# Kernel optimization log

Hardware: AMD Instinct MI355X
Metric: run time of the kernel (lower is better)

## Reference

```python
import jax, jax.numpy as jnp
import numpy as np

N = 50000       # nodes
E = 800000      # edges (avg degree 16)
D_IN = 128      # in_channels
H = 128         # hidden_channels
C = 10          # num_classes
G = 64          # graphs in batch


def setup_inputs() -> dict:
    key = jax.random.key(0)
    ks = jax.random.split(key, 9)
    x = jax.random.normal(ks[0], (N, D_IN), dtype=jnp.float32)
    edge_index = jax.random.randint(ks[1], (2, E), 0, N, dtype=jnp.int32)
    batch = jnp.sort(jax.random.randint(ks[2], (N,), 0, G, dtype=jnp.int32))
    # glorot-ish init for weights, zeros for biases (PyG GCNConv default: glorot W, zero b)
    W1 = jax.random.normal(ks[3], (D_IN, H), dtype=jnp.float32) * (1.0 / np.sqrt(D_IN))
    b1 = jnp.zeros((H,), dtype=jnp.float32)
    W2 = jax.random.normal(ks[4], (H, H), dtype=jnp.float32) * (1.0 / np.sqrt(H))
    b2 = jnp.zeros((H,), dtype=jnp.float32)
    Wc = jax.random.normal(ks[5], (H, C), dtype=jnp.float32) * (1.0 / np.sqrt(H))
    bc = jnp.zeros((C,), dtype=jnp.float32)
    return {"x": x, "edge_index": edge_index, "batch": batch,
            "W1": W1, "b1": b1, "W2": W2, "b2": b2, "Wc": Wc, "bc": bc}


def _gcn_conv(x, edge_index, W, b):
    # PyG GCNConv: add self-loops, symmetric normalization D^-1/2 (A+I) D^-1/2 (X W) + b
    loop = jnp.arange(N, dtype=edge_index.dtype)
    row = jnp.concatenate([edge_index[0], loop])  # source
    col = jnp.concatenate([edge_index[1], loop])  # target (aggregation side)
    deg = jax.ops.segment_sum(jnp.ones(row.shape[0], dtype=x.dtype), col, num_segments=N)
    dis = jax.lax.rsqrt(deg)  # deg >= 1 due to self-loops
    norm = dis[row] * dis[col]                     # [E+N]
    h = x @ W                                      # [N, H]
    msg = h[row] * norm[:, None]                   # gather + scale
    out = jax.ops.segment_sum(msg, col, num_segments=N)  # scatter-add at targets
    return out + b


def reference(x, edge_index, batch, W1, b1, W2, b2, Wc, bc):
    h = jax.nn.relu(_gcn_conv(x, edge_index, W1, b1))
    h = jax.nn.relu(_gcn_conv(h, edge_index, W2, b2))
    # global mean pool per graph
    sums = jax.ops.segment_sum(h, batch, num_segments=G)          # [G, H]
    counts = jax.ops.segment_sum(jnp.ones((N,), dtype=h.dtype), batch, num_segments=G)
    pooled = sums / jnp.maximum(counts, 1.0)[:, None]
    return pooled @ Wc + bc                                       # [G, C]
```

## Files before the change

### kernel.cpp

```cpp
#include <hip/hip_runtime.h>
#include <hip/hip_fp16.h>

typedef _Float16 half8 __attribute__((ext_vector_type(8)));
typedef float f32x4 __attribute__((ext_vector_type(4)));

#define PAD 64


__global__ __launch_bounds__(256) void fill_pad_k(const int* __restrict__ row, const int* __restrict__ col,
                                                  int* __restrict__ cnt, unsigned short* __restrict__ csr,
                                                  int E) {
    int i8 = blockIdx.x * 256 + threadIdx.x;
    int base = i8 * 8;
    if (base + 7 < E) {
        int4 r0 = ((const int4*)row)[i8 * 2];
        int4 r1 = ((const int4*)row)[i8 * 2 + 1];
        int4 c0 = ((const int4*)col)[i8 * 2];
        int4 c1 = ((const int4*)col)[i8 * 2 + 1];
        int p0 = atomicAdd(&cnt[c0.x], 1);
        int p1 = atomicAdd(&cnt[c0.y], 1);
        int p2 = atomicAdd(&cnt[c0.z], 1);
        int p3 = atomicAdd(&cnt[c0.w], 1);
        int p4 = atomicAdd(&cnt[c1.x], 1);
        int p5 = atomicAdd(&cnt[c1.y], 1);
        int p6 = atomicAdd(&cnt[c1.z], 1);
        int p7 = atomicAdd(&cnt[c1.w], 1);
        if (p0 < PAD) csr[c0.x * PAD + p0] = (unsigned short)r0.x;
        if (p1 < PAD) csr[c0.y * PAD + p1] = (unsigned short)r0.y;
        if (p2 < PAD) csr[c0.z * PAD + p2] = (unsigned short)r0.z;
        if (p3 < PAD) csr[c0.w * PAD + p3] = (unsigned short)r0.w;
        if (p4 < PAD) csr[c1.x * PAD + p4] = (unsigned short)r1.x;
        if (p5 < PAD) csr[c1.y * PAD + p5] = (unsigned short)r1.y;
        if (p6 < PAD) csr[c1.z * PAD + p6] = (unsigned short)r1.z;
        if (p7 < PAD) csr[c1.w * PAD + p7] = (unsigned short)r1.w;
    } else {
        for (int e = base; e < E; ++e) {
            int t = col[e];
            int p = atomicAdd(&cnt[t], 1);
            if (p < PAD) csr[t * PAD + p] = (unsigned short)row[e];
        }
    }
}

__global__ __launch_bounds__(256) void dis_k(const int* __restrict__ cnt, float* __restrict__ dis, int n) {
    int i = blockIdx.x * 256 + threadIdx.x;
    if (i < n) dis[i] = rsqrtf(1.0f + (float)min(cnt[i], PAD));
}


template<bool FP16IN>
__global__ __launch_bounds__(256) void gemm_mfma(const void* __restrict__ Ain,
                                                 const float* __restrict__ W,
                                                 const float* __restrict__ dis,
                                                 _Float16* __restrict__ O, int nrows) {
    int tid = threadIdx.x;
    int lane = tid & 63;
    int wave = tid >> 6;
    int wr = wave >> 1, wc = wave & 1;
    int row0 = blockIdx.x * 64 + wr * 32;
    int colbase = wc * 64;
    int lrow = lane & 15;
    int lkb = lane >> 4;

    half8 bfrag[4][4];
    #pragma unroll
    for (int ct = 0; ct < 4; ++ct) {
        int colw = colbase + ct * 16 + lrow;
        #pragma unroll
        for (int ks = 0; ks < 4; ++ks) {
            int k0 = ks * 32 + lkb * 8;
            #pragma unroll
            for (int j = 0; j < 8; ++j)
                bfrag[ct][ks][j] = (_Float16)W[(k0 + j) * 128 + colw];
        }
    }

    f32x4 acc[2][4] = {};
    #pragma unroll
    for (int ks = 0; ks < 4; ++ks) {
        int k0 = ks * 32 + lkb * 8;
        half8 afrag[2];
        #pragma unroll
        for (int rt = 0; rt < 2; ++rt) {
            int r = row0 + rt * 16 + lrow;
            r = r < nrows ? r : nrows - 1;
            if (FP16IN) {
                afrag[rt] = *reinterpret_cast<const half8*>(&((const _Float16*)Ain)[r * 128 + k0]);
            } else {
                const float4* p = reinterpret_cast<const float4*>(&((const float*)Ain)[r * 128 + k0]);
                float4 u = p[0], v = p[1];
                half8 h;
                h[0] = (_Float16)u.x; h[1] = (_Float16)u.y; h[2] = (_Float16)u.z; h[3] = (_Float16)u.w;
                h[4] = (_Float16)v.x; h[5] = (_Float16)v.y; h[6] = (_Float16)v.z; h[7] = (_Float16)v.w;
                afrag[rt] = h;
            }
        }
        #pragma unroll
        for (int rt = 0; rt < 2; ++rt)
            #pragma unroll
            for (int ct = 0; ct < 4; ++ct)
                acc[rt][ct] = __builtin_amdgcn_mfma_f32_16x16x32_f16(afrag[rt], bfrag[ct][ks],
                                                                     acc[rt][ct], 0, 0, 0);
    }

    #pragma unroll
    for (int rt = 0; rt < 2; ++rt) {
        #pragma unroll
        for (int j = 0; j < 4; ++j) {
            int r = row0 + rt * 16 + lkb * 4 + j;
            if (r < nrows) {
                float d = dis[r];
                #pragma unroll
                for (int ct = 0; ct < 4; ++ct) {
                    int colw = colbase + ct * 16 + lrow;
                    O[r * 128 + colw] = (_Float16)(acc[rt][ct][j] * d);
                }
            }
        }
    }
}


__device__ __forceinline__ float2 gather_sum(const __half2* __restrict__ h2,
                                             const unsigned short* __restrict__ src,
                                             int e, int lane, float2 a0) {
    float2 a1 = {0.f, 0.f}, a2 = {0.f, 0.f}, a3 = {0.f, 0.f};
    int i = 0;
    for (; i + 7 < e; i += 8) {
        int s0 = src[i],     s1 = src[i + 1], s2 = src[i + 2], s3 = src[i + 3];
        int s4 = src[i + 4], s5 = src[i + 5], s6 = src[i + 6], s7 = src[i + 7];
        float2 v0 = __half22float2(h2[s0 * 64 + lane]);
        float2 v1 = __half22float2(h2[s1 * 64 + lane]);
        float2 v2 = __half22float2(h2[s2 * 64 + lane]);
        float2 v3 = __half22float2(h2[s3 * 64 + lane]);
        float2 v4 = __half22float2(h2[s4 * 64 + lane]);
        float2 v5 = __half22float2(h2[s5 * 64 + lane]);
        float2 v6 = __half22float2(h2[s6 * 64 + lane]);
        float2 v7 = __half22float2(h2[s7 * 64 + lane]);
        a0.x += v0.x; a0.y += v0.y;
        a1.x += v1.x; a1.y += v1.y;
        a2.x += v2.x; a2.y += v2.y;
        a3.x += v3.x; a3.y += v3.y;
        a0.x += v4.x; a0.y += v4.y;
        a1.x += v5.x; a1.y += v5.y;
        a2.x += v6.x; a2.y += v6.y;
        a3.x += v7.x; a3.y += v7.y;
    }
    for (; i + 3 < e; i += 4) {
        int s0 = src[i], s1 = src[i + 1], s2 = src[i + 2], s3 = src[i + 3];
        float2 v0 = __half22float2(h2[s0 * 64 + lane]);
        float2 v1 = __half22float2(h2[s1 * 64 + lane]);
        float2 v2 = __half22float2(h2[s2 * 64 + lane]);
        float2 v3 = __half22float2(h2[s3 * 64 + lane]);
        a0.x += v0.x; a0.y += v0.y;
        a1.x += v1.x; a1.y += v1.y;
        a2.x += v2.x; a2.y += v2.y;
        a3.x += v3.x; a3.y += v3.y;
    }
    for (; i < e; ++i) {
        float2 v0 = __half22float2(h2[src[i] * 64 + lane]);
        a0.x += v0.x; a0.y += v0.y;
    }
    float2 r;
    r.x = a0.x + a1.x + a2.x + a3.x;
    r.y = a0.y + a1.y + a2.y + a3.y;
    return r;
}

__global__ __launch_bounds__(256) void agg_k(const _Float16* __restrict__ h, const int* __restrict__ cnt,
                                             const unsigned short* __restrict__ csr_pad,
                                             const float* __restrict__ dis,
                                             const float* __restrict__ bias,
                                             _Float16* __restrict__ out, int n) {
    int wave = threadIdx.x >> 6;
    int lane = threadIdx.x & 63;
    int node = blockIdx.x * 4 + wave;
    if (node >= n) return;
    const __half2* h2 = (const __half2*)h;
    float2 self = __half22float2(h2[node * 64 + lane]);
    int deg = min(cnt[node], PAD);
    float2 a = gather_sum(h2, csr_pad + node * PAD, deg, lane, self);
    float d = dis[node];
    float2 bb = ((const float2*)bias)[lane];
    float vx = a.x * d + bb.x;
    float vy = a.y * d + bb.y;
    ((__half2*)out)[node * 64 + lane] = __floats2half2_rn(fmaxf(vx, 0.f), fmaxf(vy, 0.f));
}


__global__ __launch_bounds__(256) void agg_pool_k(const _Float16* __restrict__ h,
                                                  const int* __restrict__ cnt,
                                                  const unsigned short* __restrict__ csr_pad,
                                                  const float* __restrict__ dis,
                                                  const float* __restrict__ bias,
                                                  const int* __restrict__ batch,
                                                  float* __restrict__ sums, int n) {
    int wave = threadIdx.x >> 6;
    int lane = threadIdx.x & 63;
    int node0 = (blockIdx.x * 4 + wave) * 4;
    if (node0 >= n) return;
    const __half2* h2 = (const __half2*)h;
    float2 bb = ((const float2*)bias)[lane];
    float2 pool = {0.f, 0.f};
    int curg = batch[node0];
    #pragma unroll
    for (int k = 0; k < 4; ++k) {
        int node = node0 + k;
        if (node >= n) break;
        float2 self = __half22float2(h2[node * 64 + lane]);
        int deg = min(cnt[node], PAD);
        float2 a = gather_sum(h2, csr_pad + node * PAD, deg, lane, self);
        float d = dis[node];
        float vx = fmaxf(a.x * d + bb.x, 0.f);
        float vy = fmaxf(a.y * d + bb.y, 0.f);
        int g = batch[node];
        if (g != curg) {
            atomicAdd(&sums[curg * 128 + lane * 2], pool.x);
            atomicAdd(&sums[curg * 128 + lane * 2 + 1], pool.y);
            pool.x = 0.f; pool.y = 0.f;
            curg = g;
        }
        pool.x += vx;
        pool.y += vy;
    }
    atomicAdd(&sums[curg * 128 + lane * 2], pool.x);
    atomicAdd(&sums[curg * 128 + lane * 2 + 1], pool.y);
}


__global__ __launch_bounds__(256) void bounds_k(const int* __restrict__ batch, int* __restrict__ start,
                                                int n, int g) {
    int i = blockIdx.x * 256 + threadIdx.x;
    if (i >= n) return;
    int b = batch[i];
    int bp = (i == 0) ? -1 : batch[i - 1];
    for (int q = bp + 1; q <= b; ++q) start[q] = i;
    if (i == n - 1) for (int q = b + 1; q <= g; ++q) start[q] = n;
}

__global__ __launch_bounds__(128) void final_k(const float* __restrict__ sums, const int* __restrict__ start,
                                               const float* __restrict__ Wc, const float* __restrict__ bc,
                                               float* __restrict__ outp, int C) {
    __shared__ float sp[128];
    int g = blockIdx.x;
    int t = threadIdx.x;
    float cntf = fmaxf((float)(start[g + 1] - start[g]), 1.0f);
    sp[t] = sums[g * 128 + t] / cntf;
    __syncthreads();
    if (t < C) {
        float acc = bc[t];
        #pragma unroll 8
        for (int cc = 0; cc < 128; ++cc) acc += sp[cc] * Wc[cc * C + t];
        outp[g * C + t] = acc;
    }
}


extern "C" void kernel_launch(void* const* d_in, const int* in_sizes, int n_in,
                              void* d_out, int out_size, void* d_ws, size_t ws_size,
                              hipStream_t stream) {
    const float* x    = (const float*)d_in[0];
    const int*   ei   = (const int*)d_in[1];
    const int*   batch= (const int*)d_in[2];
    const float* W1   = (const float*)d_in[3];
    const float* b1   = (const float*)d_in[4];
    const float* W2   = (const float*)d_in[5];
    const float* b2   = (const float*)d_in[6];
    const float* Wc   = (const float*)d_in[7];
    const float* bc   = (const float*)d_in[8];

    const int N = in_sizes[0] / 128;
    const int E = in_sizes[1] / 2;
    const int C = in_sizes[7] / 128;
    const int G = out_size / C;

    const int* row = ei;
    const int* col = ei + E;

    char* ws = (char*)d_ws;
    size_t o = 0;
    auto take = [&](size_t nbytes) -> char* {
        char* p = ws + o;
        o = (o + nbytes + 255) & ~(size_t)255;
        return p;
    };
    int*   cnt     = (int*)take((size_t)N * 4);
    float* sums    = (float*)take((size_t)G * 128 * 4);
    size_t zero_span = o;
    float* dis     = (float*)take((size_t)N * 4);
    int*   start   = (int*)take((size_t)(G + 1) * 4);
    unsigned short* csr_pad = (unsigned short*)take((size_t)N * PAD * 2);
    _Float16* bufA = (_Float16*)take((size_t)N * 128 * 2);
    _Float16* bufB = (_Float16*)take((size_t)N * 128 * 2);

    hipMemsetAsync(d_ws, 0, zero_span, stream);

    int gE8 = (E / 8 + 255) / 256;
    int gN = (N + 255) / 256;

    fill_pad_k<<<gE8, 256, 0, stream>>>(row, col, cnt, csr_pad, E);
    dis_k<<<gN, 256, 0, stream>>>(cnt, dis, N);

    int gGemm = (N + 63) / 64;
    int gAgg  = (N + 3) / 4;
    int gAggP = (N + 15) / 16;

    gemm_mfma<false><<<gGemm, 256, 0, stream>>>((const void*)x, W1, dis, bufA, N);
    agg_k<<<gAgg, 256, 0, stream>>>(bufA, cnt, csr_pad, dis, b1, bufB, N);
    gemm_mfma<true><<<gGemm, 256, 0, stream>>>((const void*)bufB, W2, dis, bufA, N);
    agg_pool_k<<<gAggP, 256, 0, stream>>>(bufA, cnt, csr_pad, dis, b2, batch, sums, N);

    bounds_k<<<gN, 256, 0, stream>>>(batch, start, N, G);
    final_k<<<G, 128, 0, stream>>>(sums, start, Wc, bc, (float*)d_out, C);
}
```

Baseline: 175.8 us.

## Gather rows with 16-byte vector loads over four nodes per wave

Both aggregation kernels now assign four nodes to each wave. Each 16-lane quarter handles an edge slot and loads 8 fp16 features at once with a 16-byte load. Partial sums are combined across lanes with xor shuffles. The self-loop is moved into the padded CSR as slot 0 by a new init kernel, and a zero row N serves as the target for masked-out edge slots. The aim is more memory-level parallelism and wider loads in the gather-bound aggregation. The cost is extra shuffle reductions and padded work up to the maximum degree in each group of four nodes. Putting the self-loop inside the 64-slot pad also means one fewer real neighbour fits per node.

Result: slower. 309.4 us (+76.0%).

```diff
diff --git a/kernel.cpp b/kernel.cpp
--- a/kernel.cpp
+++ b/kernel.cpp
@@ -1,10 +1,22 @@
 #include <hip/hip_runtime.h>
 #include <hip/hip_fp16.h>
 
+typedef _Float16 half8v __attribute__((ext_vector_type(8)));
+typedef float f32x4 __attribute__((ext_vector_type(4)));
 typedef _Float16 half8 __attribute__((ext_vector_type(8)));
-typedef float f32x4 __attribute__((ext_vector_type(4)));
 
 #define PAD 64
+
+
+__global__ __launch_bounds__(256) void csr_init_k(int* __restrict__ cnt, unsigned short* __restrict__ csr,
+                                                  _Float16* __restrict__ rowN, int n) {
+    int i = blockIdx.x * 256 + threadIdx.x;
+    if (i < n) {
+        cnt[i] = 1;
+        csr[(size_t)i * PAD] = (unsigned short)i;
+    }
+    if (blockIdx.x == 0 && threadIdx.x < 128) rowN[threadIdx.x] = (_Float16)0.f;
+}
 
 
 __global__ __launch_bounds__(256) void fill_pad_k(const int* __restrict__ row, const int* __restrict__ col,
@@ -44,7 +56,7 @@
 
 __global__ __launch_bounds__(256) void dis_k(const int* __restrict__ cnt, float* __restrict__ dis, int n) {
     int i = blockIdx.x * 256 + threadIdx.x;
-    if (i < n) dis[i] = rsqrtf(1.0f + (float)min(cnt[i], PAD));
+    if (i < n) dis[i] = rsqrtf((float)min(cnt[i], PAD));
 }
 
 
@@ -121,110 +133,132 @@
 }
 
 
-__device__ __forceinline__ float2 gather_sum(const __half2* __restrict__ h2,
-                                             const unsigned short* __restrict__ src,
-                                             int e, int lane, float2 a0) {
-    float2 a1 = {0.f, 0.f}, a2 = {0.f, 0.f}, a3 = {0.f, 0.f};
-    int i = 0;
-    for (; i + 7 < e; i += 8) {
-        int s0 = src[i],     s1 = src[i + 1], s2 = src[i + 2], s3 = src[i + 3];
-        int s4 = src[i + 4], s5 = src[i + 5], s6 = src[i + 6], s7 = src[i + 7];
-        float2 v0 = __half22float2(h2[s0 * 64 + lane]);
-        float2 v1 = __half22float2(h2[s1 * 64 + lane]);
-        float2 v2 = __half22float2(h2[s2 * 64 + lane]);
-        float2 v3 = __half22float2(h2[s3 * 64 + lane]);
-        float2 v4 = __half22float2(h2[s4 * 64 + lane]);
-        float2 v5 = __half22float2(h2[s5 * 64 + lane]);
-        float2 v6 = __half22float2(h2[s6 * 64 + lane]);
-        float2 v7 = __half22float2(h2[s7 * 64 + lane]);
-        a0.x += v0.x; a0.y += v0.y;
-        a1.x += v1.x; a1.y += v1.y;
-        a2.x += v2.x; a2.y += v2.y;
-        a3.x += v3.x; a3.y += v3.y;
-        a0.x += v4.x; a0.y += v4.y;
-        a1.x += v5.x; a1.y += v5.y;
-        a2.x += v6.x; a2.y += v6.y;
-        a3.x += v7.x; a3.y += v7.y;
-    }
-    for (; i + 3 < e; i += 4) {
-        int s0 = src[i], s1 = src[i + 1], s2 = src[i + 2], s3 = src[i + 3];
-        float2 v0 = __half22float2(h2[s0 * 64 + lane]);
-        float2 v1 = __half22float2(h2[s1 * 64 + lane]);
-        float2 v2 = __half22float2(h2[s2 * 64 + lane]);
-        float2 v3 = __half22float2(h2[s3 * 64 + lane]);
-        a0.x += v0.x; a0.y += v0.y;
-        a1.x += v1.x; a1.y += v1.y;
-        a2.x += v2.x; a2.y += v2.y;
-        a3.x += v3.x; a3.y += v3.y;
-    }
-    for (; i < e; ++i) {
-        float2 v0 = __half22float2(h2[src[i] * 64 + lane]);
-        a0.x += v0.x; a0.y += v0.y;
-    }
-    float2 r;
-    r.x = a0.x + a1.x + a2.x + a3.x;
-    r.y = a0.y + a1.y + a2.y + a3.y;
-    return r;
-}
+__device__ __forceinline__ void gather4(const _Float16* __restrict__ h,
+                                        const unsigned short* __restrict__ csr,
+                                        const int* __restrict__ cnt,
+                                        int node0, int n, int q, int p,
+                                        float acc[4][8]) {
+    int deg[4];
+    const unsigned short* base[4];
+    #pragma unroll
+    for (int j = 0; j < 4; ++j) {
+        int nd = node0 + j;
+        bool v = nd < n;
+        deg[j] = v ? min(cnt[nd], PAD) : 0;
+        base[j] = csr + (size_t)(v ? nd : 0) * PAD;
+    }
+    int maxdeg = max(max(deg[0], deg[1]), max(deg[2], deg[3]));
+    for (int i = 0; i < maxdeg; i += 8) {
+        #pragma unroll
+        for (int j = 0; j < 4; ++j) {
+            int ea = i + q, eb = i + 4 + q;
+            int ia = base[j][ea];
+            int ib = base[j][eb];
+            ia = ea < deg[j] ? ia : n;
+            ib = eb < deg[j] ? ib : n;
+            half8v va = *reinterpret_cast<const half8v*>(h + (size_t)ia * 128 + p * 8);
+            half8v vb = *reinterpret_cast<const half8v*>(h + (size_t)ib * 128 + p * 8);
+            #pragma unroll
+            for (int c = 0; c < 8; ++c)
+                acc[j][c] += (float)va[c] + (float)vb[c];
+        }
+    }
+}
+
+__device__ __forceinline__ void reduce8(float a[8]) {
+    #pragma unroll
+    for (int c = 0; c < 8; ++c) {
+        float t = a[c];
+        t += __shfl_xor(t, 16);
+        t += __shfl_xor(t, 32);
+        a[c] = t;
+    }
+}
+
 
 __global__ __launch_bounds__(256) void agg_k(const _Float16* __restrict__ h, const int* __restrict__ cnt,
-                                             const unsigned short* __restrict__ csr_pad,
+                                             const unsigned short* __restrict__ csr,
                                              const float* __restrict__ dis,
                                              const float* __restrict__ bias,
                                              _Float16* __restrict__ out, int n) {
     int wave = threadIdx.x >> 6;
     int lane = threadIdx.x & 63;
-    int node = blockIdx.x * 4 + wave;
-    if (node >= n) return;
-    const __half2* h2 = (const __half2*)h;
-    float2 self = __half22float2(h2[node * 64 + lane]);
-    int deg = min(cnt[node], PAD);
-    float2 a = gather_sum(h2, csr_pad + node * PAD, deg, lane, self);
-    float d = dis[node];
-    float2 bb = ((const float2*)bias)[lane];
-    float vx = a.x * d + bb.x;
-    float vy = a.y * d + bb.y;
-    ((__half2*)out)[node * 64 + lane] = __floats2half2_rn(fmaxf(vx, 0.f), fmaxf(vy, 0.f));
+    int q = lane >> 4, p = lane & 15;
+    int node0 = (blockIdx.x * 4 + wave) * 4;
+    if (node0 >= n) return;
+
+    float acc[4][8] = {};
+    gather4(h, csr, cnt, node0, n, q, p, acc);
+
+    float4 bb0 = ((const float4*)bias)[p * 2];
+    float4 bb1 = ((const float4*)bias)[p * 2 + 1];
+    float bb[8] = {bb0.x, bb0.y, bb0.z, bb0.w, bb1.x, bb1.y, bb1.z, bb1.w};
+
+    #pragma unroll
+    for (int j = 0; j < 4; ++j) {
+        int nd = node0 + j;
+        if (nd >= n) continue;
+        reduce8(acc[j]);
+        float d = dis[nd];
+        if (q == j) {
+            half8v o;
+            #pragma unroll
+            for (int c = 0; c < 8; ++c)
+                o[c] = (_Float16)fmaxf(acc[j][c] * d + bb[c], 0.f);
+            *reinterpret_cast<half8v*>(out + (size_t)nd * 128 + p * 8) = o;
+        }
+    }
 }
 
 
 __global__ __launch_bounds__(256) void agg_pool_k(const _Float16* __restrict__ h,
                                                   const int* __restrict__ cnt,
-                                                  const unsigned short* __restrict__ csr_pad,
+                                                  const unsigned short* __restrict__ csr,
                                                   const float* __restrict__ dis,
                                                   const float* __restrict__ bias,
                                                   const int* __restrict__ batch,
                                                   float* __restrict__ sums, int n) {
     int wave = threadIdx.x >> 6;
     int lane = threadIdx.x & 63;
+    int q = lane >> 4, p = lane & 15;
     int node0 = (blockIdx.x * 4 + wave) * 4;
     if (node0 >= n) return;
-    const __half2* h2 = (const __half2*)h;
-    float2 bb = ((const float2*)bias)[lane];
-    float2 pool = {0.f, 0.f};
+
+    float acc[4][8] = {};
+    gather4(h, csr, cnt, node0, n, q, p, acc);
+
+    float4 bb0 = ((const float4*)bias)[p * 2];
+    float4 bb1 = ((const float4*)bias)[p * 2 + 1];
+    float bb[8] = {bb0.x, bb0.y, bb0.z, bb0.w, bb1.x, bb1.y, bb1.z, bb1.w};
+
+    float pool[8] = {};
     int curg = batch[node0];
     #pragma unroll
-    for (int k = 0; k < 4; ++k) {
-        int node = node0 + k;
-        if (node >= n) break;
-        float2 self = __half22float2(h2[node * 64 + lane]);
-        int deg = min(cnt[node], PAD);
-        float2 a = gather_sum(h2, csr_pad + node * PAD, deg, lane, self);
-        float d = dis[node];
-        float vx = fmaxf(a.x * d + bb.x, 0.f);
-        float vy = fmaxf(a.y * d + bb.y, 0.f);
-        int g = batch[node];
+    for (int j = 0; j < 4; ++j) {
+        int nd = node0 + j;
+        if (nd >= n) continue;
+        reduce8(acc[j]);
+        int g = batch[nd];
         if (g != curg) {
-            atomicAdd(&sums[curg * 128 + lane * 2], pool.x);
-            atomicAdd(&sums[curg * 128 + lane * 2 + 1], pool.y);
-            pool.x = 0.f; pool.y = 0.f;
+            if (lane < 16) {
+                #pragma unroll
+                for (int c = 0; c < 8; ++c)
+                    atomicAdd(&sums[curg * 128 + p * 8 + c], pool[c]);
+            }
+            #pragma unroll
+            for (int c = 0; c < 8; ++c) pool[c] = 0.f;
             curg = g;
         }
-        pool.x += vx;
-        pool.y += vy;
-    }
-    atomicAdd(&sums[curg * 128 + lane * 2], pool.x);
-    atomicAdd(&sums[curg * 128 + lane * 2 + 1], pool.y);
+        float d = dis[nd];
+        #pragma unroll
+        for (int c = 0; c < 8; ++c)
+            pool[c] += fmaxf(acc[j][c] * d + bb[c], 0.f);
+    }
+    if (lane < 16) {
+        #pragma unroll
+        for (int c = 0; c < 8; ++c)
+            atomicAdd(&sums[curg * 128 + p * 8 + c], pool[c]);
+    }
 }
 
 
@@ -284,13 +318,13 @@
         o = (o + nbytes + 255) & ~(size_t)255;
         return p;
     };
-    int*   cnt     = (int*)take((size_t)N * 4);
     float* sums    = (float*)take((size_t)G * 128 * 4);
     size_t zero_span = o;
+    int*   cnt     = (int*)take((size_t)N * 4);
     float* dis     = (float*)take((size_t)N * 4);
     int*   start   = (int*)take((size_t)(G + 1) * 4);
     unsigned short* csr_pad = (unsigned short*)take((size_t)N * PAD * 2);
-    _Float16* bufA = (_Float16*)take((size_t)N * 128 * 2);
+    _Float16* bufA = (_Float16*)take((size_t)(N + 1) * 128 * 2);
     _Float16* bufB = (_Float16*)take((size_t)N * 128 * 2);
 
     hipMemsetAsync(d_ws, 0, zero_span, stream);
@@ -298,17 +332,17 @@
     int gE8 = (E / 8 + 255) / 256;
     int gN = (N + 255) / 256;
 
+    csr_init_k<<<gN, 256, 0, stream>>>(cnt, csr_pad, bufA + (size_t)N * 128, N);
     fill_pad_k<<<gE8, 256, 0, stream>>>(row, col, cnt, csr_pad, E);
     dis_k<<<gN, 256, 0, stream>>>(cnt, dis, N);
 
     int gGemm = (N + 63) / 64;
-    int gAgg  = (N + 3) / 4;
-    int gAggP = (N + 15) / 16;
+    int gAgg  = (N + 15) / 16;
 
     gemm_mfma<false><<<gGemm, 256, 0, stream>>>((const void*)x, W1, dis, bufA, N);
     agg_k<<<gAgg, 256, 0, stream>>>(bufA, cnt, csr_pad, dis, b1, bufB, N);
     gemm_mfma<true><<<gGemm, 256, 0, stream>>>((const void*)bufB, W2, dis, bufA, N);
-    agg_pool_k<<<gAggP, 256, 0, stream>>>(bufA, cnt, csr_pad, dis, b2, batch, sums, N);
+    agg_pool_k<<<gAgg, 256, 0, stream>>>(bufA, cnt, csr_pad, dis, b2, batch, sums, N);
 
     bounds_k<<<gN, 256, 0, stream>>>(batch, start, N, G);
     final_k<<<G, 128, 0, stream>>>(sums, start, Wc, bc, (float*)d_out, C);
```

## Split CSR fill atomics across two counter arrays and compact afterwards

Applied to the files above, without the earlier changes.

Edge insertion now spreads its atomics over two counter arrays, one per half of each 8-edge chunk. Each counter writes into its own 32-slot half of the padded row, and a compaction pass then merges the two halves. The self-loop is stored as the first CSR entry during init, so the aggregation kernels no longer load the self feature separately. The aim is to halve atomic contention on hot counters, at the cost of two extra small kernels and a per-node compaction loop. Nodes with more than 32 in-edges in either half silently drop edges, and the self-loop takes one of the 32 first-half slots.

Result: no change. 179.1 us (+1.9%).

```diff
diff --git a/kernel.cpp b/kernel.cpp
--- a/kernel.cpp
+++ b/kernel.cpp
@@ -7,9 +7,20 @@
 #define PAD 64
 
 
-__global__ __launch_bounds__(256) void fill_pad_k(const int* __restrict__ row, const int* __restrict__ col,
-                                                  int* __restrict__ cnt, unsigned short* __restrict__ csr,
-                                                  int E) {
+__global__ __launch_bounds__(256) void csr_init_k(int* __restrict__ cnt0, int* __restrict__ cnt1,
+                                                  unsigned short* __restrict__ csr, int n) {
+    int i = blockIdx.x * 256 + threadIdx.x;
+    if (i < n) {
+        cnt0[i] = 1;
+        cnt1[i] = 0;
+        csr[(size_t)i * PAD] = (unsigned short)i;
+    }
+}
+
+
+__global__ __launch_bounds__(256) void fill2_k(const int* __restrict__ row, const int* __restrict__ col,
+                                               int* __restrict__ cnt0, int* __restrict__ cnt1,
+                                               unsigned short* __restrict__ csr, int E) {
     int i8 = blockIdx.x * 256 + threadIdx.x;
     int base = i8 * 8;
     if (base + 7 < E) {
@@ -17,34 +28,43 @@
         int4 r1 = ((const int4*)row)[i8 * 2 + 1];
         int4 c0 = ((const int4*)col)[i8 * 2];
         int4 c1 = ((const int4*)col)[i8 * 2 + 1];
-        int p0 = atomicAdd(&cnt[c0.x], 1);
-        int p1 = atomicAdd(&cnt[c0.y], 1);
-        int p2 = atomicAdd(&cnt[c0.z], 1);
-        int p3 = atomicAdd(&cnt[c0.w], 1);
-        int p4 = atomicAdd(&cnt[c1.x], 1);
-        int p5 = atomicAdd(&cnt[c1.y], 1);
-        int p6 = atomicAdd(&cnt[c1.z], 1);
-        int p7 = atomicAdd(&cnt[c1.w], 1);
-        if (p0 < PAD) csr[c0.x * PAD + p0] = (unsigned short)r0.x;
-        if (p1 < PAD) csr[c0.y * PAD + p1] = (unsigned short)r0.y;
-        if (p2 < PAD) csr[c0.z * PAD + p2] = (unsigned short)r0.z;
-        if (p3 < PAD) csr[c0.w * PAD + p3] = (unsigned short)r0.w;
-        if (p4 < PAD) csr[c1.x * PAD + p4] = (unsigned short)r1.x;
-        if (p5 < PAD) csr[c1.y * PAD + p5] = (unsigned short)r1.y;
-        if (p6 < PAD) csr[c1.z * PAD + p6] = (unsigned short)r1.z;
-        if (p7 < PAD) csr[c1.w * PAD + p7] = (unsigned short)r1.w;
+        int p0 = atomicAdd(&cnt0[c0.x], 1);
+        int p1 = atomicAdd(&cnt0[c0.y], 1);
+        int p2 = atomicAdd(&cnt0[c0.z], 1);
+        int p3 = atomicAdd(&cnt0[c0.w], 1);
+        int p4 = atomicAdd(&cnt1[c1.x], 1);
+        int p5 = atomicAdd(&cnt1[c1.y], 1);
+        int p6 = atomicAdd(&cnt1[c1.z], 1);
+        int p7 = atomicAdd(&cnt1[c1.w], 1);
+        if (p0 < 32) csr[c0.x * PAD + p0] = (unsigned short)r0.x;
+        if (p1 < 32) csr[c0.y * PAD + p1] = (unsigned short)r0.y;
+        if (p2 < 32) csr[c0.z * PAD + p2] = (unsigned short)r0.z;
+        if (p3 < 32) csr[c0.w * PAD + p3] = (unsigned short)r0.w;
+        if (p4 < 32) csr[c1.x * PAD + 32 + p4] = (unsigned short)r1.x;
+        if (p5 < 32) csr[c1.y * PAD + 32 + p5] = (unsigned short)r1.y;
+        if (p6 < 32) csr[c1.z * PAD + 32 + p6] = (unsigned short)r1.z;
+        if (p7 < 32) csr[c1.w * PAD + 32 + p7] = (unsigned short)r1.w;
     } else {
         for (int e = base; e < E; ++e) {
             int t = col[e];
-            int p = atomicAdd(&cnt[t], 1);
-            if (p < PAD) csr[t * PAD + p] = (unsigned short)row[e];
-        }
-    }
-}
-
-__global__ __launch_bounds__(256) void dis_k(const int* __restrict__ cnt, float* __restrict__ dis, int n) {
+            int p = atomicAdd(&cnt0[t], 1);
+            if (p < 32) csr[t * PAD + p] = (unsigned short)row[e];
+        }
+    }
+}
+
+
+__global__ __launch_bounds__(256) void compact_k(int* __restrict__ cnt0, const int* __restrict__ cnt1,
+                                                 unsigned short* __restrict__ csr,
+                                                 float* __restrict__ dis, int n) {
     int i = blockIdx.x * 256 + threadIdx.x;
-    if (i < n) dis[i] = rsqrtf(1.0f + (float)min(cnt[i], PAD));
+    if (i >= n) return;
+    int c0 = min(cnt0[i], 32);
+    int c1 = min(cnt1[i], 32);
+    unsigned short* b = csr + (size_t)i * PAD;
+    for (int k = 0; k < c1; ++k) b[c0 + k] = b[32 + k];
+    cnt0[i] = c0 + c1;
+    dis[i] = rsqrtf((float)(c0 + c1));
 }
 
 
@@ -123,8 +143,8 @@
 
 __device__ __forceinline__ float2 gather_sum(const __half2* __restrict__ h2,
                                              const unsigned short* __restrict__ src,
-                                             int e, int lane, float2 a0) {
-    float2 a1 = {0.f, 0.f}, a2 = {0.f, 0.f}, a3 = {0.f, 0.f};
+                                             int e, int lane) {
+    float2 a0 = {0.f, 0.f}, a1 = {0.f, 0.f}, a2 = {0.f, 0.f}, a3 = {0.f, 0.f};
     int i = 0;
     for (; i + 7 < e; i += 8) {
         int s0 = src[i],     s1 = src[i + 1], s2 = src[i + 2], s3 = src[i + 3];
@@ -167,8 +187,9 @@
     return r;
 }
 
+
 __global__ __launch_bounds__(256) void agg_k(const _Float16* __restrict__ h, const int* __restrict__ cnt,
-                                             const unsigned short* __restrict__ csr_pad,
+                                             const unsigned short* __restrict__ csr,
                                              const float* __restrict__ dis,
                                              const float* __restrict__ bias,
                                              _Float16* __restrict__ out, int n) {
@@ -177,9 +198,8 @@
     int node = blockIdx.x * 4 + wave;
     if (node >= n) return;
     const __half2* h2 = (const __half2*)h;
-    float2 self = __half22float2(h2[node * 64 + lane]);
-    int deg = min(cnt[node], PAD);
-    float2 a = gather_sum(h2, csr_pad + node * PAD, deg, lane, self);
+    int deg = cnt[node];
+    float2 a = gather_sum(h2, csr + (size_t)node * PAD, deg, lane);
     float d = dis[node];
     float2 bb = ((const float2*)bias)[lane];
     float vx = a.x * d + bb.x;
@@ -190,7 +210,7 @@
 
 __global__ __launch_bounds__(256) void agg_pool_k(const _Float16* __restrict__ h,
                                                   const int* __restrict__ cnt,
-                                                  const unsigned short* __restrict__ csr_pad,
+                                                  const unsigned short* __restrict__ csr,
                                                   const float* __restrict__ dis,
                                                   const float* __restrict__ bias,
                                                   const int* __restrict__ batch,
@@ -207,9 +227,8 @@
     for (int k = 0; k < 4; ++k) {
         int node = node0 + k;
         if (node >= n) break;
-        float2 self = __half22float2(h2[node * 64 + lane]);
-        int deg = min(cnt[node], PAD);
-        float2 a = gather_sum(h2, csr_pad + node * PAD, deg, lane, self);
+        int deg = cnt[node];
+        float2 a = gather_sum(h2, csr + (size_t)node * PAD, deg, lane);
         float d = dis[node];
         float vx = fmaxf(a.x * d + bb.x, 0.f);
         float vy = fmaxf(a.y * d + bb.y, 0.f);
@@ -284,9 +303,10 @@
         o = (o + nbytes + 255) & ~(size_t)255;
         return p;
     };
-    int*   cnt     = (int*)take((size_t)N * 4);
     float* sums    = (float*)take((size_t)G * 128 * 4);
     size_t zero_span = o;
+    int*   cnt0    = (int*)take((size_t)N * 4);
+    int*   cnt1    = (int*)take((size_t)N * 4);
     float* dis     = (float*)take((size_t)N * 4);
     int*   start   = (int*)take((size_t)(G + 1) * 4);
     unsigned short* csr_pad = (unsigned short*)take((size_t)N * PAD * 2);
@@ -298,17 +318,18 @@
     int gE8 = (E / 8 + 255) / 256;
     int gN = (N + 255) / 256;
 
-    fill_pad_k<<<gE8, 256, 0, stream>>>(row, col, cnt, csr_pad, E);
-    dis_k<<<gN, 256, 0, stream>>>(cnt, dis, N);
-
-    int gGemm = (N + 63) / 64;
-    int gAgg  = (N + 3) / 4;
-    int gAggP = (N + 15) / 16;
+    csr_init_k<<<gN, 256, 0, stream>>>(cnt0, cnt1, csr_pad, N);
+    fill2_k<<<gE8, 256, 0, stream>>>(row, col, cnt0, cnt1, csr_pad, E);
+    compact_k<<<gN, 256, 0, stream>>>(cnt0, cnt1, csr_pad, dis, N);
+
+    int gGemm  = (N + 63) / 64;
+    int gAgg1  = (N + 3) / 4;
+    int gAggP  = (N + 15) / 16;
 
     gemm_mfma<false><<<gGemm, 256, 0, stream>>>((const void*)x, W1, dis, bufA, N);
-    agg_k<<<gAgg, 256, 0, stream>>>(bufA, cnt, csr_pad, dis, b1, bufB, N);
+    agg_k<<<gAgg1, 256, 0, stream>>>(bufA, cnt0, csr_pad, dis, b1, bufB, N);
     gemm_mfma<true><<<gGemm, 256, 0, stream>>>((const void*)bufB, W2, dis, bufA, N);
-    agg_pool_k<<<gAggP, 256, 0, stream>>>(bufA, cnt, csr_pad, dis, b2, batch, sums, N);
+    agg_pool_k<<<gAggP, 256, 0, stream>>>(bufA, cnt0, csr_pad, dis, b2, batch, sums, N);
 
     bounds_k<<<gN, 256, 0, stream>>>(batch, start, N, G);
     final_k<<<G, 128, 0, stream>>>(sums, start, Wc, bc, (float*)d_out, C);
```
